# Performance work log

Hardware: AMD Instinct MI355X
Metric: run time of the kernel (lower is better)

Reference implementation:

```python
import jax, jax.numpy as jnp
import numpy as np

B, N, C, T = 2048, 512, 64, 128  # batch, codebook size, latent channels, latent time


def setup_inputs() -> dict:
    key = jax.random.key(0)
    k1, k2 = jax.random.split(key)
    y = jax.random.normal(k1, (B, C, T), dtype=jnp.float32)   # encoder latents
    m = jax.random.normal(k2, (N, C, T), dtype=jnp.float32)   # centroid means
    sd = jnp.ones((N, C, T), dtype=jnp.float32)               # centroid variances
    p = jnp.zeros((N,), dtype=jnp.float32) + 1e-6             # cluster counts
    return {"y": y, "m": m, "sd": sd, "p": p}


def reference(y, m, sd, p):
    # --- squared-distance argmin assignment (same math as (y-m)^2 summed over C,T) ---
    b = y.shape[0]
    yf = y.reshape(b, -1)                 # [B, D]
    mf = m.reshape(m.shape[0], -1)        # [N, D]
    d2 = (yf * yf).sum(-1)[:, None] + (mf * mf).sum(-1)[None, :] - 2.0 * (yf @ mf.T)
    assign = jnp.argmin(d2, axis=1)       # [B] int assignments

    # --- sequential, order-sensitive EMA scatter updates (faithful to python loop) ---
    def step(carry, inp):
        p_, m_, sd_ = carry
        yi, zi = inp
        p_ = p_.at[zi].add(1.0)
        mi = m_[zi] * 0.001 + yi * 0.999
        m_ = m_.at[zi].set(mi)
        sdi = (mi - yi) ** 2 * 0.001 + sd_[zi] * 0.999
        sd_ = sd_.at[zi].set(sdi)
        return (p_, m_, sd_), None

    (p, m, sd), _ = jax.lax.scan(step, (p, m, sd), (y, assign))
    return m, sd, p, assign
```

## Files before the change

### kernel.cpp

```cpp
#include <hip/hip_runtime.h>
#include <hip/hip_bf16.h>


#define Bb 2048
#define Nn 512
#define Dd 8192
#define MARGIN 12.0f
#define KC 8
#define KSTEPS 32

typedef __attribute__((ext_vector_type(4))) float f32x4;
typedef __attribute__((ext_vector_type(8))) short s16x8;

union Frag { unsigned u[4]; s16x8 s; };

__device__ inline unsigned pack2(float lo, float hi) {
    return __builtin_amdgcn_perm(__float_as_uint(hi), __float_as_uint(lo), 0x07060302u);
}

__device__ inline void ema4(float4& mcv, float4& scv, const float4 yv) {
#define EMA_C(c) { mcv.c = mcv.c * 0.001f + yv.c * 0.999f; \
                   float d_ = mcv.c - yv.c;                 \
                   scv.c = d_ * d_ * 0.001f + scv.c * 0.999f; }
    EMA_C(x) EMA_C(y) EMA_C(z) EMA_C(w)
#undef EMA_C
}

__global__ __launch_bounds__(256) void m_norms(const float* __restrict__ M,
                                               float* __restrict__ mm) {
    int n = blockIdx.x, t = threadIdx.x;
    const float4* r = (const float4*)(M + (size_t)n * Dd);
    float s = 0.f;
#pragma unroll
    for (int u = 0; u < 8; u++) {
        float4 v = r[t + 256 * u];
        s += v.x * v.x + v.y * v.y + v.z * v.z + v.w * v.w;
    }
    __shared__ float red[256];
    red[t] = s;
    __syncthreads();
    for (int off = 128; off > 0; off >>= 1) {
        if (t < off) red[t] += red[t + off];
        __syncthreads();
    }
    if (t == 0) mm[n] = red[0];
}

__global__ __launch_bounds__(512, 4) void gemm_coarse(const float* __restrict__ Y,
                                                      const float* __restrict__ M,
                                                      float* __restrict__ part) {
    __shared__ __align__(16) float As[128 * 32];
    __shared__ __align__(16) float Bs[128 * 32];
    const int t = threadIdx.x;
    const int lane = t & 63;
    const int w = t >> 6;
    const int ct = blockIdx.x, rt = blockIdx.y, kc = blockIdx.z;

    const size_t ybase = (size_t)rt * 128 * Dd + (size_t)kc * (KSTEPS * 32);
    const size_t mbase = (size_t)ct * 128 * Dd + (size_t)kc * (KSTEPS * 32);

    int rowS[2], soff[2];
#pragma unroll
    for (int u = 0; u < 2; u++) {
        int flat = (w * 2 + u) * 64 + lane;
        int row = flat >> 3, seg = flat & 7;
        rowS[u] = row;
        soff[u] = (seg ^ (row & 7)) * 4;
    }

    const int wr0 = (w & 3) * 32, wc0 = (w >> 2) * 64;
    const int l15 = lane & 15, quad = lane >> 4;

    f32x4 acc[2][4];
#pragma unroll
    for (int i = 0; i < 2; i++)
#pragma unroll
        for (int j = 0; j < 4; j++) acc[i][j] = (f32x4)(0.0f);

    for (int step = 0; step < KSTEPS; step++) {
        const int kpos = step * 32;
#pragma unroll
        for (int u = 0; u < 2; u++) {
            const float* gA = Y + ybase + (size_t)rowS[u] * Dd + kpos + soff[u];
            const float* gB = M + mbase + (size_t)rowS[u] * Dd + kpos + soff[u];
            __builtin_amdgcn_global_load_lds(
                (const __attribute__((address_space(1))) void*)gA,
                (__attribute__((address_space(3))) void*)(As + (w * 2 + u) * 256), 16, 0, 0);
            __builtin_amdgcn_global_load_lds(
                (const __attribute__((address_space(1))) void*)gB,
                (__attribute__((address_space(3))) void*)(Bs + (w * 2 + u) * 256), 16, 0, 0);
        }
        __syncthreads();

        Frag fa[2], fb[4];
#pragma unroll
        for (int ta = 0; ta < 2; ta++) {
            int rowa = wr0 + ta * 16 + l15;
            const float* Ar = As + rowa * 32;
            int s0 = ((quad * 2) ^ (rowa & 7)) * 4;
            int s1 = ((quad * 2 + 1) ^ (rowa & 7)) * 4;
            f32x4 x0 = *(const f32x4*)(Ar + s0);
            f32x4 x1 = *(const f32x4*)(Ar + s1);
            fa[ta].u[0] = pack2(x0[0], x0[1]);
            fa[ta].u[1] = pack2(x0[2], x0[3]);
            fa[ta].u[2] = pack2(x1[0], x1[1]);
            fa[ta].u[3] = pack2(x1[2], x1[3]);
        }
#pragma unroll
        for (int tb = 0; tb < 4; tb++) {
            int rowb = wc0 + tb * 16 + l15;
            const float* Br = Bs + rowb * 32;
            int s0 = ((quad * 2) ^ (rowb & 7)) * 4;
            int s1 = ((quad * 2 + 1) ^ (rowb & 7)) * 4;
            f32x4 x0 = *(const f32x4*)(Br + s0);
            f32x4 x1 = *(const f32x4*)(Br + s1);
            fb[tb].u[0] = pack2(x0[0], x0[1]);
            fb[tb].u[1] = pack2(x0[2], x0[3]);
            fb[tb].u[2] = pack2(x1[0], x1[1]);
            fb[tb].u[3] = pack2(x1[2], x1[3]);
        }
#pragma unroll
        for (int i = 0; i < 2; i++)
#pragma unroll
            for (int j = 0; j < 4; j++)
                acc[i][j] = __builtin_amdgcn_mfma_f32_16x16x32_bf16(fa[i].s, fb[j].s, acc[i][j], 0, 0, 0);
        __syncthreads();
    }

    float* P = part + (size_t)kc * (Bb * Nn);
#pragma unroll
    for (int i = 0; i < 2; i++) {
        int rg = rt * 128 + wr0 + i * 16 + quad * 4;
#pragma unroll
        for (int j = 0; j < 4; j++) {
            int cg = ct * 128 + wc0 + j * 16 + l15;
#pragma unroll
            for (int r = 0; r < 4; r++)
                P[(size_t)(rg + r) * Nn + cg] = acc[i][j][r];
        }
    }
}

__global__ __launch_bounds__(256) void rescore(const float* __restrict__ Y,
                                               const float* __restrict__ M,
                                               const float* __restrict__ part,
                                               const float* __restrict__ mm,
                                               float* __restrict__ assignF) {
    __shared__ float redW[4];
    __shared__ int candList[Nn];
    __shared__ float candD2[Nn];
    __shared__ int candCnt;
    int b = blockIdx.x, t = threadIdx.x, lane = t & 63, w = t >> 6;
    if (t == 0) candCnt = 0;

    int c0 = t, c1 = t + 256;
    float dot0 = 0.f, dot1 = 0.f;
#pragma unroll
    for (int k = 0; k < KC; k++) {
        dot0 += part[(size_t)k * (Bb * Nn) + (size_t)b * Nn + c0];
        dot1 += part[(size_t)k * (Bb * Nn) + (size_t)b * Nn + c1];
    }
    float d0 = mm[c0] - 2.0f * dot0;
    float d1 = mm[c1] - 2.0f * dot1;

    float mn = fminf(d0, d1);
#pragma unroll
    for (int off = 32; off > 0; off >>= 1) mn = fminf(mn, __shfl_xor(mn, off));
    if (lane == 0) redW[w] = mn;
    __syncthreads();
    float thresh = fminf(fminf(redW[0], redW[1]), fminf(redW[2], redW[3])) + MARGIN;

    if (d0 <= thresh) candList[atomicAdd(&candCnt, 1)] = c0;
    if (d1 <= thresh) candList[atomicAdd(&candCnt, 1)] = c1;
    __syncthreads();
    int ncand = candCnt;

    if (ncand == 1) {
        if (t == 0) assignF[b] = (float)candList[0];
        return;
    }

    const float4* yr = (const float4*)(Y + (size_t)b * Dd);
    for (int j = w; j < ncand; j += 4) {
        int c = candList[j];
        const float4* mr = (const float4*)(M + (size_t)c * Dd);
        float p = 0.f;
#pragma unroll 8
        for (int u = 0; u < 32; u++) {
            float4 yv = yr[u * 64 + lane];
            float4 mv = mr[u * 64 + lane];
            p += yv.x * mv.x + yv.y * mv.y + yv.z * mv.z + yv.w * mv.w;
        }
#pragma unroll
        for (int off = 32; off > 0; off >>= 1) p += __shfl_xor(p, off);
        if (lane == 0) candD2[j] = mm[c] - 2.0f * p;
    }
    __syncthreads();

    if (t == 0) {
        float bestV = 3.4e38f;
        int bestI = 0x3fffffff;
        for (int j = 0; j < ncand; j++) {
            float d2e = candD2[j];
            int c = candList[j];
            if (d2e < bestV || (d2e == bestV && c < bestI)) { bestV = d2e; bestI = c; }
        }
        assignF[b] = (float)bestI;
    }
}

__global__ __launch_bounds__(256) void ema_scatter(const float* __restrict__ Y,
                                                   const float* __restrict__ M0,
                                                   const float* __restrict__ SD0,
                                                   const float* __restrict__ P0,
                                                   const float* __restrict__ assignF,
                                                   float* __restrict__ m_out,
                                                   float* __restrict__ sd_out,
                                                   float* __restrict__ p_out) {
    __shared__ int lst[Bb];
    __shared__ int cntSh;
    int n = blockIdx.x, s = blockIdx.y, t = threadIdx.x, lane = t & 63, w = t >> 6;

    if (w == 0) {
        int cnt = 0;
#pragma unroll
        for (int u = 0; u < 32; u++) {
            int zi = (int)assignF[u * 64 + lane];
            unsigned long long mask = __ballot(zi == n);
            if (zi == n) lst[cnt + (int)__popcll(mask & ((1ull << lane) - 1ull))] = u * 64 + lane;
            cnt += (int)__popcll(mask);
        }
        if (lane == 0) {
            cntSh = cnt;
            if (s == 0) p_out[n] = P0[n] + (float)cnt;
        }
    }
    __syncthreads();
    int cnt = cntSh;

    size_t off = (size_t)n * Dd + (size_t)s * 1024;
    float4 mc = *(const float4*)(M0 + off + 4 * t);
    float4 sc = *(const float4*)(SD0 + off + 4 * t);

    int j = 0;
    for (; j + 16 <= cnt; j += 16) {
        float4 yv[16];
#pragma unroll
        for (int q = 0; q < 16; q++)
            yv[q] = *(const float4*)(Y + (size_t)lst[j + q] * Dd + (size_t)s * 1024 + 4 * t);
#pragma unroll
        for (int q = 0; q < 16; q++) ema4(mc, sc, yv[q]);
    }
    for (; j < cnt; j++) {
        float4 yv = *(const float4*)(Y + (size_t)lst[j] * Dd + (size_t)s * 1024 + 4 * t);
        ema4(mc, sc, yv);
    }

    *(float4*)(m_out + off + 4 * t) = mc;
    *(float4*)(sd_out + off + 4 * t) = sc;
}

extern "C" void kernel_launch(void* const* d_in, const int* in_sizes, int n_in,
                              void* d_out, int out_size, void* d_ws, size_t ws_size,
                              hipStream_t stream) {
    const float* y  = (const float*)d_in[0];
    const float* m  = (const float*)d_in[1];
    const float* sd = (const float*)d_in[2];
    const float* p  = (const float*)d_in[3];

    float* out     = (float*)d_out;
    float* m_out   = out;
    float* sd_out  = out + 4194304;
    float* p_out   = out + 8388608;
    float* assignF = out + 8389120;
    float* part    = out;

    m_norms    <<<Nn, 256, 0, stream>>>(m, p_out);
    gemm_coarse<<<dim3(4, 16, KC), 512, 0, stream>>>(y, m, part);
    rescore    <<<Bb, 256, 0, stream>>>(y, m, part, p_out, assignF);
    ema_scatter<<<dim3(Nn, 8), 256, 0, stream>>>(y, m, sd, p, assignF, m_out, sd_out, p_out);
}
```

Before: 226.3 us.

## Double-buffer LDS tiles in coarse GEMM and remap block order

The coarse bf16 GEMM now uses two LDS buffers per operand, so the async global-to-LDS loads for the next K-step are issued before the MFMA compute on the current one. This aims to hide global load latency behind compute. The 3D grid is also flattened to 1D, with the K-chunk index in the low bits so blocks sharing the same Y/M rows run close together, which may improve L2 reuse. LDS use per block doubles to 64 KB, which could lower occupancy below the 4 blocks the launch bounds request.

```diff
diff --git a/kernel.cpp b/kernel.cpp
--- a/kernel.cpp
+++ b/kernel.cpp
@@ -49,12 +49,16 @@
 __global__ __launch_bounds__(512, 4) void gemm_coarse(const float* __restrict__ Y,
                                                       const float* __restrict__ M,
                                                       float* __restrict__ part) {
-    __shared__ __align__(16) float As[128 * 32];
-    __shared__ __align__(16) float Bs[128 * 32];
+    __shared__ __align__(16) float As[2][128 * 32];
+    __shared__ __align__(16) float Bs[2][128 * 32];
     const int t = threadIdx.x;
     const int lane = t & 63;
     const int w = t >> 6;
-    const int ct = blockIdx.x, rt = blockIdx.y, kc = blockIdx.z;
+
+    const int bid = blockIdx.x;
+    const int kc = bid & 7;
+    const int ct = (bid >> 3) & 3;
+    const int rt = bid >> 5;
 
     const size_t ybase = (size_t)rt * 128 * Dd + (size_t)kc * (KSTEPS * 32);
     const size_t mbase = (size_t)ct * 128 * Dd + (size_t)kc * (KSTEPS * 32);
@@ -77,7 +81,7 @@
 #pragma unroll
         for (int j = 0; j < 4; j++) acc[i][j] = (f32x4)(0.0f);
 
-    for (int step = 0; step < KSTEPS; step++) {
+    auto stage = [&](int buf, int step) {
         const int kpos = step * 32;
 #pragma unroll
         for (int u = 0; u < 2; u++) {
@@ -85,18 +89,19 @@
             const float* gB = M + mbase + (size_t)rowS[u] * Dd + kpos + soff[u];
             __builtin_amdgcn_global_load_lds(
                 (const __attribute__((address_space(1))) void*)gA,
-                (__attribute__((address_space(3))) void*)(As + (w * 2 + u) * 256), 16, 0, 0);
+                (__attribute__((address_space(3))) void*)(&As[buf][0] + (w * 2 + u) * 256), 16, 0, 0);
             __builtin_amdgcn_global_load_lds(
                 (const __attribute__((address_space(1))) void*)gB,
-                (__attribute__((address_space(3))) void*)(Bs + (w * 2 + u) * 256), 16, 0, 0);
-        }
-        __syncthreads();
-
+                (__attribute__((address_space(3))) void*)(&Bs[buf][0] + (w * 2 + u) * 256), 16, 0, 0);
+        }
+    };
+
+    auto compute = [&](int buf) {
         Frag fa[2], fb[4];
 #pragma unroll
         for (int ta = 0; ta < 2; ta++) {
             int rowa = wr0 + ta * 16 + l15;
-            const float* Ar = As + rowa * 32;
+            const float* Ar = &As[buf][0] + rowa * 32;
             int s0 = ((quad * 2) ^ (rowa & 7)) * 4;
             int s1 = ((quad * 2 + 1) ^ (rowa & 7)) * 4;
             f32x4 x0 = *(const f32x4*)(Ar + s0);
@@ -109,7 +114,7 @@
 #pragma unroll
         for (int tb = 0; tb < 4; tb++) {
             int rowb = wc0 + tb * 16 + l15;
-            const float* Br = Bs + rowb * 32;
+            const float* Br = &Bs[buf][0] + rowb * 32;
             int s0 = ((quad * 2) ^ (rowb & 7)) * 4;
             int s1 = ((quad * 2 + 1) ^ (rowb & 7)) * 4;
             f32x4 x0 = *(const f32x4*)(Br + s0);
@@ -124,6 +129,16 @@
 #pragma unroll
             for (int j = 0; j < 4; j++)
                 acc[i][j] = __builtin_amdgcn_mfma_f32_16x16x32_bf16(fa[i].s, fb[j].s, acc[i][j], 0, 0, 0);
+    };
+
+    stage(0, 0);
+    __syncthreads();
+    for (int step = 0; step < KSTEPS; step += 2) {
+        stage(1, step + 1);
+        compute(0);
+        __syncthreads();
+        if (step + 2 < KSTEPS) stage(0, step + 2);
+        compute(1);
         __syncthreads();
     }
 
@@ -276,7 +291,7 @@
     float* part    = out;
 
     m_norms    <<<Nn, 256, 0, stream>>>(m, p_out);
-    gemm_coarse<<<dim3(4, 16, KC), 512, 0, stream>>>(y, m, part);
+    gemm_coarse<<<dim3(512), 512, 0, stream>>>(y, m, part);
     rescore    <<<Bb, 256, 0, stream>>>(y, m, part, p_out, assignF);
     ema_scatter<<<dim3(Nn, 8), 256, 0, stream>>>(y, m, sd, p, assignF, m_out, sd_out, p_out);
 }
```

After: 218.8 us. -3.3%, faster.
